# Kernel optimization log

Hardware: AMD Instinct MI355X
Metric: run time of the kernel (lower is better)

The kernel has to match this reference:

```python
import jax, jax.numpy as jnp
import numpy as np

B, C_IN, C_OUT, C_KEY, N = 8, 512, 512, 256, 2048


def setup_inputs() -> dict:
    key = jax.random.key(0)
    k1, k2, k3, k4 = jax.random.split(key, 4)
    x = jax.random.normal(k1, (B, C_IN, N), dtype=jnp.float32)
    # Conv1d(kernel=1, bias=False) weights -> plain linear maps over channel dim
    Wq = jax.random.normal(k2, (C_KEY, C_IN), dtype=jnp.float32) * (1.0 / np.sqrt(C_IN))
    Wk = jax.random.normal(k3, (C_KEY, C_IN), dtype=jnp.float32) * (1.0 / np.sqrt(C_IN))
    Wv = jax.random.normal(k4, (C_OUT, C_IN), dtype=jnp.float32) * (1.0 / np.sqrt(C_IN))
    return {"x": x, "Wq": Wq, "Wk": Wk, "Wv": Wv}


def reference(x, Wq, Wk, Wv):
    # 1x1 conv projections: [B, C, N] -> [B, Ck/Co, N]
    q = jnp.einsum("oc,bcn->bon", Wq, x)
    k = jnp.einsum("oc,bcn->bon", Wk, x)
    v = jnpqv = jnp.einsum("oc,bcn->bon", Wv, x)
    # sim_map[b,i,j] = sum_c k[b,c,i] * q[b,c,j]  (unscaled)
    sim = jnp.einsum("bci,bcj->bij", k, q)  # [B, N, N]
    attn = jax.nn.softmax(sim, axis=-1)
    # out = value @ sim_map, then permute(0,2,1) -> [B, N, C_out]
    out = jnp.einsum("bck,bkm->bmc", jnpqv, attn)
    return out
```

## Files before the change

kernel.cpp:

```cpp
#include <hip/hip_runtime.h>

typedef _Float16 half8 __attribute__((ext_vector_type(8)));
typedef _Float16 half4v __attribute__((ext_vector_type(4)));
typedef _Float16 half2v __attribute__((ext_vector_type(2)));
typedef float f32x4 __attribute__((ext_vector_type(4)));

#define ASYNC_CP16(gp, lp)                                       \
  __builtin_amdgcn_global_load_lds(                              \
      (const __attribute__((address_space(1))) void*)(gp),       \
      (__attribute__((address_space(3))) void*)(lp), 16, 0, 0)

static __device__ __forceinline__ half8 mulw(half8 a, half8 s) {
  half8 o;
#pragma unroll
  for (int j = 0; j < 8; j++) o[j] = a[j] * s[j];
  return o;
}

__global__ __launch_bounds__(256) void conv_w(const float* __restrict__ Wq,
                                              const float* __restrict__ Wk,
                                              const float* __restrict__ Wv,
                                              _Float16* __restrict__ Wb) {
  int idx = blockIdx.x * 256 + threadIdx.x;
  int row = idx >> 9;
  float v;
  if (row < 256)      v = Wq[idx];
  else if (row < 512) v = Wk[idx - 256 * 512];
  else                v = Wv[idx - 512 * 512];
  Wb[idx] = (_Float16)v;
}

__global__ __launch_bounds__(256) void conv_xT(const float* __restrict__ x,
                                               _Float16* __restrict__ xT) {
  __shared__ float T[32][33];
  const int b = blockIdx.z;
  const int n0 = blockIdx.x * 32, c0 = blockIdx.y * 32;
  const int t = threadIdx.x;
  const float* xb = x + (size_t)b * 512 * 2048;
  const int n2 = t & 15, cr = t >> 4;
#pragma unroll
  for (int r = 0; r < 2; r++) {
    int c = cr + r * 16;
    float2 v = *(const float2*)&xb[(size_t)(c0 + c) * 2048 + n0 + n2 * 2];
    T[c][n2 * 2] = v.x;
    T[c][n2 * 2 + 1] = v.y;
  }
  __syncthreads();
  _Float16* xtb = xT + (size_t)b * 2048 * 512;
  const int c2 = t & 15, nr = t >> 4;
#pragma unroll
  for (int r = 0; r < 2; r++) {
    int n = nr + r * 16;
    half2v h;
    h[0] = (_Float16)T[c2 * 2][n];
    h[1] = (_Float16)T[c2 * 2 + 1][n];
    *(half2v*)&xtb[(size_t)(n0 + n) * 512 + c0 + c2 * 2] = h;
  }
}

#define STAGE_NT(bb, kbase)                                   \
  ASYNC_CP16(gA + (kbase), &As[bb][0][wofs]);                 \
  ASYNC_CP16(gA + (kbase) + 32, &As[bb][1][wofs]);            \
  ASYNC_CP16(gB + (kbase), &Bs[bb][0][wofs]);                 \
  ASYNC_CP16(gB2 + (kbase), &Bs[bb][0][4096 + wofs]);         \
  ASYNC_CP16(gB + (kbase) + 32, &Bs[bb][1][wofs]);            \
  ASYNC_CP16(gB2 + (kbase) + 32, &Bs[bb][1][4096 + wofs]);

template <int MODE, int NT>
__global__ __launch_bounds__(512) void gemm_nt(
    const _Float16* __restrict__ A, const _Float16* __restrict__ B,
    _Float16* __restrict__ C, _Float16* __restrict__ C2, int lda, int ldb,
    int ldc, int ldc2, long sA, long sB, long sC, float* __restrict__ pm,
    float* __restrict__ ps) {
  A += (size_t)blockIdx.z * sA;
  B += (size_t)blockIdx.z * sB;
  C += (size_t)blockIdx.z * sC;
  if constexpr (MODE == 1) C2 += (size_t)blockIdx.z * sC;
  const int m_blk = blockIdx.y * 128, n_blk = blockIdx.x * 256;

  __shared__ __align__(16) _Float16 As[3][2][4096];
  __shared__ __align__(16) _Float16 Bs[3][2][8192];

  const int t = threadIdx.x;
  const int lane = t & 63, wave = t >> 6;
  const int quad = lane >> 4, l16 = lane & 15;
  const int wm = (wave & 1) * 64, wn = (wave >> 1) * 64;

  const int arow = t >> 2, aslot = t & 3;
  const int adc = aslot ^ ((arow >> 1) & 3);
  const _Float16* gA = A + (size_t)(m_blk + arow) * lda + adc * 8;
  const _Float16* gB = B + (size_t)(n_blk + arow) * ldb + adc * 8;
  const _Float16* gB2 = gB + (size_t)128 * ldb;
  const int wofs = wave * 512 + lane * 8;

  const int rchunk = (quad ^ ((l16 >> 1) & 3)) * 8;

  f32x4 acc[4][4] = {};

  STAGE_NT(0, 0);
  STAGE_NT(1, 64);
  asm volatile("s_waitcnt vmcnt(6)\n\ts_barrier" ::: "memory");
  __builtin_amdgcn_sched_barrier(0);

  int cbuf = 0;
  for (int T = 0; T < NT; T++) {
    const int kb2 = (T + 2) * 64;
    half8 af[4], bf[4];
#pragma unroll
    for (int i = 0; i < 4; i++) {
      af[i] = *(const half8*)&As[cbuf][0][(wm + i * 16 + l16) * 32 + rchunk];
      bf[i] = *(const half8*)&Bs[cbuf][0][(wn + i * 16 + l16) * 32 + rchunk];
    }
    if (T + 2 < NT) {
      int nb = cbuf + 2;
      if (nb >= 3) nb -= 3;
      STAGE_NT(nb, kb2);
    }
    asm volatile("s_barrier" ::: "memory");
    __builtin_amdgcn_sched_barrier(0);
    __builtin_amdgcn_s_setprio(1);
#pragma unroll
    for (int i = 0; i < 4; i++)
#pragma unroll
      for (int j = 0; j < 4; j++)
        acc[i][j] =
            __builtin_amdgcn_mfma_f32_16x16x32_f16(af[i], bf[j], acc[i][j], 0, 0, 0);
    __builtin_amdgcn_s_setprio(0);
    asm volatile("s_barrier" ::: "memory");
    __builtin_amdgcn_sched_barrier(0);
    half8 af2[4], bf2[4];
#pragma unroll
    for (int i = 0; i < 4; i++) {
      af2[i] = *(const half8*)&As[cbuf][1][(wm + i * 16 + l16) * 32 + rchunk];
      bf2[i] = *(const half8*)&Bs[cbuf][1][(wn + i * 16 + l16) * 32 + rchunk];
    }
    if (T + 2 < NT)
      asm volatile("s_waitcnt vmcnt(6)\n\ts_barrier" ::: "memory");
    else
      asm volatile("s_waitcnt vmcnt(0)\n\ts_barrier" ::: "memory");
    __builtin_amdgcn_sched_barrier(0);
    __builtin_amdgcn_s_setprio(1);
#pragma unroll
    for (int i = 0; i < 4; i++)
#pragma unroll
      for (int j = 0; j < 4; j++)
        acc[i][j] =
            __builtin_amdgcn_mfma_f32_16x16x32_f16(af2[i], bf2[j], acc[i][j], 0, 0, 0);
    __builtin_amdgcn_s_setprio(0);
    asm volatile("s_barrier" ::: "memory");
    __builtin_amdgcn_sched_barrier(0);
    cbuf++;
    if (cbuf == 3) cbuf = 0;
  }

  if constexpr (MODE == 2) {
#pragma unroll
    for (int j = 0; j < 4; j++) {
      const int n0 = n_blk + wn + j * 16 + l16;
      float mx = acc[0][j][0];
#pragma unroll
      for (int i = 0; i < 4; i++)
#pragma unroll
        for (int r = 0; r < 4; r++) mx = fmaxf(mx, acc[i][j][r]);
      mx = fmaxf(mx, __shfl_xor(mx, 16, 64));
      mx = fmaxf(mx, __shfl_xor(mx, 32, 64));
      float es = 0.f;
#pragma unroll
      for (int i = 0; i < 4; i++) {
        const int m0 = m_blk + wm + i * 16 + quad * 4;
#pragma unroll
        for (int r = 0; r < 4; r++) {
          _Float16 h = (_Float16)__expf(acc[i][j][r] - mx);
          C[(size_t)(m0 + r) * ldc + n0] = h;
          es += (float)h;
        }
      }
      es += __shfl_xor(es, 16, 64);
      es += __shfl_xor(es, 32, 64);
      if (quad == 0) {
        size_t o = ((size_t)blockIdx.z * 32 + blockIdx.y * 2 + (wave & 1)) *
                       2048 + n0;
        pm[o] = mx;
        ps[o] = es;
      }
    }
  } else {
#pragma unroll
    for (int i = 0; i < 4; i++) {
      const int m0 = m_blk + wm + i * 16 + quad * 4;
#pragma unroll
      for (int j = 0; j < 4; j++) {
        const int n0 = n_blk + wn + j * 16 + l16;
        if (m_blk < 512) {
          half4v h;
#pragma unroll
          for (int r = 0; r < 4; r++) h[r] = (_Float16)acc[i][j][r];
          *(half4v*)&C[(size_t)n0 * ldc + m0] = h;
        } else {
#pragma unroll
          for (int r = 0; r < 4; r++)
            C2[(size_t)(m0 - 512 + r) * ldc2 + n0] = (_Float16)acc[i][j][r];
        }
      }
    }
  }
}

__global__ __launch_bounds__(256) void colstats2(const float* __restrict__ pm,
                                                 const float* __restrict__ ps,
                                                 _Float16* __restrict__ scl) {
  const int idx = blockIdx.x * 256 + threadIdx.x;
  const int b = idx >> 11, col = idx & 2047;
  const float* pmb = pm + (size_t)b * 32 * 2048 + col;
  const float* psb = ps + (size_t)b * 32 * 2048 + col;
  float pv[32];
  float m = -3.0e38f;
#pragma unroll
  for (int i = 0; i < 32; i++) {
    pv[i] = pmb[(size_t)i * 2048];
    m = fmaxf(m, pv[i]);
  }
  float s = 0.f;
#pragma unroll
  for (int i = 0; i < 32; i++) {
    pv[i] = __expf(pv[i] - m);
    s += psb[(size_t)i * 2048] * pv[i];
  }
  const float inv = 1.0f / s;
  _Float16* so = scl + (size_t)b * 32 * 2048 + col;
#pragma unroll
  for (int i = 0; i < 32; i++) so[(size_t)i * 2048] = (_Float16)(pv[i] * inv);
}

__global__ __launch_bounds__(512) void gemm_av(const _Float16* __restrict__ P,
                                               const _Float16* __restrict__ V,
                                               const _Float16* __restrict__ scl,
                                               float* __restrict__ C,
                                               int cbatch) {
  int lin = blockIdx.x, z, idx;
  if (cbatch == 8) {
    z = lin & 7;
    idx = lin >> 3;
  } else {
    z = lin >> 5;
    idx = lin & 31;
  }
  const int n_blk = (idx & 1) * 256;
  const int m_blk = (idx >> 1) * 128;
  P += (size_t)z * 2048 * 2048;
  V += (size_t)z * 512 * 2048;
  scl += (size_t)z * 32 * 2048;
  C += (size_t)z * 2048 * 512;

  __shared__ __align__(16) _Float16 Asv[2][2][4096];
  __shared__ __align__(16) _Float16 Bsv[2][2][8192];

  const int t = threadIdx.x;
  const int lane = t & 63, wave = t >> 6;
  const int quad = lane >> 4, l16 = lane & 15;
  const int wm = (wave & 1) * 64, wn = (wave >> 1) * 64;

  const int arow = t >> 2;
  const int aslot = t & 3;
  const int adc = aslot ^ ((arow >> 1) & 3);
  const _Float16* gA = P + (size_t)(m_blk + arow) * 2048 + adc * 8;
  const _Float16* gS = scl + (size_t)((m_blk + arow) >> 6) * 2048 + adc * 8;
  const int awofs = arow * 32 + aslot * 8;

  const int brow0 = (wave << 4) + (lane >> 2);
  const int bdc = (lane & 3) ^ ((brow0 >> 1) & 3);
  const _Float16* gB = V + (size_t)(n_blk + brow0) * 2048 + bdc * 8;
  const int bwofs = wave << 9;

  const int rchunk = (quad ^ ((l16 >> 1) & 3)) * 8;

  f32x4 acc[4][4] = {};

  ASYNC_CP16(gB, &Bsv[0][0][bwofs]);
  ASYNC_CP16(gB + (size_t)128 * 2048, &Bsv[0][0][4096 + bwofs]);
  ASYNC_CP16(gB + 32, &Bsv[0][1][bwofs]);
  ASYNC_CP16(gB + (size_t)128 * 2048 + 32, &Bsv[0][1][4096 + bwofs]);
  {
    half8 a00 = *(const half8*)(gA);
    half8 s00 = *(const half8*)(gS);
    half8 a01 = *(const half8*)(gA + 32);
    half8 s01 = *(const half8*)(gS + 32);
    *(half8*)&Asv[0][0][awofs] = mulw(a00, s00);
    *(half8*)&Asv[0][1][awofs] = mulw(a01, s01);
  }
  half8 pA0 = *(const half8*)(gA + 64);
  half8 pS0 = *(const half8*)(gS + 64);
  half8 pA1 = *(const half8*)(gA + 96);
  half8 pS1 = *(const half8*)(gS + 96);
  asm volatile("s_waitcnt vmcnt(4) lgkmcnt(0)\n\ts_barrier" ::: "memory");
  __builtin_amdgcn_sched_barrier(0);

  for (int T = 0; T < 32; T++) {
    const int c = T & 1, n = c ^ 1;
    const int k1 = (T + 1) * 64;
    const int k2 = (T + 2) * 64;
    half8 af[4], bf[4];
#pragma unroll
    for (int i = 0; i < 4; i++) {
      af[i] = *(const half8*)&Asv[c][0][(wm + i * 16 + l16) * 32 + rchunk];
      bf[i] = *(const half8*)&Bsv[c][0][(wn + i * 16 + l16) * 32 + rchunk];
    }
    if (T < 31) {
      ASYNC_CP16(gB + k1, &Bsv[n][0][bwofs]);
      ASYNC_CP16(gB + (size_t)128 * 2048 + k1, &Bsv[n][0][4096 + bwofs]);
      ASYNC_CP16(gB + k1 + 32, &Bsv[n][1][bwofs]);
      ASYNC_CP16(gB + (size_t)128 * 2048 + k1 + 32, &Bsv[n][1][4096 + bwofs]);
      *(half8*)&Asv[n][0][awofs] = mulw(pA0, pS0);
    }
    asm volatile("s_barrier" ::: "memory");
    __builtin_amdgcn_sched_barrier(0);
    __builtin_amdgcn_s_setprio(1);
#pragma unroll
    for (int i = 0; i < 4; i++)
#pragma unroll
      for (int j = 0; j < 4; j++)
        acc[i][j] =
            __builtin_amdgcn_mfma_f32_16x16x32_f16(af[i], bf[j], acc[i][j], 0, 0, 0);
    __builtin_amdgcn_s_setprio(0);
    asm volatile("s_barrier" ::: "memory");
    __builtin_amdgcn_sched_barrier(0);
    half8 af2[4], bf2[4];
#pragma unroll
    for (int i = 0; i < 4; i++) {
      af2[i] = *(const half8*)&Asv[c][1][(wm + i * 16 + l16) * 32 + rchunk];
      bf2[i] = *(const half8*)&Bsv[c][1][(wn + i * 16 + l16) * 32 + rchunk];
    }
    half8 fA0, fS0, fA1, fS1;
    if (T < 30) {
      fA0 = *(const half8*)(gA + k2);
      fS0 = *(const half8*)(gS + k2);
      fA1 = *(const half8*)(gA + k2 + 32);
      fS1 = *(const half8*)(gS + k2 + 32);
    }
    if (T < 31) *(half8*)&Asv[n][1][awofs] = mulw(pA1, pS1);
    if (T < 30) {
      pA0 = fA0;
      pS0 = fS0;
      pA1 = fA1;
      pS1 = fS1;
    }
    if (T < 30)
      asm volatile("s_waitcnt vmcnt(4) lgkmcnt(0)\n\ts_barrier" ::: "memory");
    else
      asm volatile("s_waitcnt vmcnt(0) lgkmcnt(0)\n\ts_barrier" ::: "memory");
    __builtin_amdgcn_sched_barrier(0);
    __builtin_amdgcn_s_setprio(1);
#pragma unroll
    for (int i = 0; i < 4; i++)
#pragma unroll
      for (int j = 0; j < 4; j++)
        acc[i][j] =
            __builtin_amdgcn_mfma_f32_16x16x32_f16(af2[i], bf2[j], acc[i][j], 0, 0, 0);
    __builtin_amdgcn_s_setprio(0);
    asm volatile("s_barrier" ::: "memory");
    __builtin_amdgcn_sched_barrier(0);
  }

#pragma unroll
  for (int i = 0; i < 4; i++) {
    const int m0 = m_blk + wm + i * 16 + quad * 4;
#pragma unroll
    for (int j = 0; j < 4; j++) {
      const int n0 = n_blk + wn + j * 16 + l16;
#pragma unroll
      for (int r = 0; r < 4; r++) C[(size_t)(m0 + r) * 512 + n0] = acc[i][j][r];
    }
  }
}

extern "C" void kernel_launch(void* const* d_in, const int* in_sizes, int n_in,
                              void* d_out, int out_size, void* d_ws,
                              size_t ws_size, hipStream_t stream) {
  const float* x = (const float*)d_in[0];
  const float* Wq = (const float*)d_in[1];
  const float* Wk = (const float*)d_in[2];
  const float* Wv = (const float*)d_in[3];
  float* out = (float*)d_out;

  char* p = (char*)d_ws;
  auto alloc = [&](size_t bytes) -> char* {
    char* r = p;
    p += (bytes + 255) & ~(size_t)255;
    return r;
  };
  const size_t NB = 8, N = 2048, CIN = 512, CO = 512;
  _Float16* Wb = (_Float16*)alloc(1024 * 512 * sizeof(_Float16));
  _Float16* xT = (_Float16*)alloc(NB * N * CIN * sizeof(_Float16));
  _Float16* qkT = (_Float16*)alloc(NB * N * 512 * sizeof(_Float16));
  _Float16* v = (_Float16*)alloc(NB * CO * N * sizeof(_Float16));
  size_t base_used = (size_t)(p - (char*)d_ws);

  const size_t per_b =
      (size_t)N * N * 2 + 2 * 32 * N * 4 + 32 * N * 2 + 8192;
  int cb = 8;
  while (cb > 1 && base_used + (size_t)cb * per_b > ws_size) cb >>= 1;
  _Float16* simH = (_Float16*)alloc((size_t)cb * N * N * 2);
  float* pm = (float*)alloc((size_t)cb * 32 * N * 4);
  float* ps = (float*)alloc((size_t)cb * 32 * N * 4);
  _Float16* scl = (_Float16*)alloc((size_t)cb * 32 * N * 2);

  conv_w<<<dim3(1024 * 512 / 256), 256, 0, stream>>>(Wq, Wk, Wv, Wb);
  conv_xT<<<dim3(64, 16, 8), 256, 0, stream>>>(x, xT);

  gemm_nt<1, 8><<<dim3(8, 8, 8), 512, 0, stream>>>(
      Wb, xT, qkT, v, 512, 512, 512, 2048, 0, (long)(N * CIN),
      (long)(N * 512), nullptr, nullptr);

  for (int b0 = 0; b0 < 8; b0 += cb) {
    const _Float16* qT = qkT + (size_t)b0 * N * 512;
    const _Float16* kT = qkT + (size_t)b0 * N * 512 + 256;
    gemm_nt<2, 4><<<dim3(8, 16, cb), 512, 0, stream>>>(
        qT, kT, simH, nullptr, 512, 512, 2048, 0, (long)(N * 512),
        (long)(N * 512), (long)(N * N), pm, ps);
    colstats2<<<dim3(cb * 8), 256, 0, stream>>>(pm, ps, scl);
    gemm_av<<<dim3(32 * cb), 512, 0, stream>>>(
        simH, v + (size_t)b0 * CO * N, scl, out + (size_t)b0 * N * CO, cb);
  }
}
```

Baseline: 202.9 us.

## Split sim GEMM into dedicated 128x128-tile kernel with 256 threads

The similarity GEMM (K=256) gets its own kernel instead of sharing the templated projection GEMM. It uses 128x128 tiles with 4 waves, a simpler triple-buffered async LDS pipeline and twice as many blocks. The goal is better occupancy and load balance on a short-K GEMM, at the cost of less operand reuse per block. The fused exp and column-stat epilogue is kept unchanged.

```diff
diff --git a/kernel.cpp b/kernel.cpp
--- a/kernel.cpp
+++ b/kernel.cpp
@@ -66,16 +66,15 @@
   ASYNC_CP16(gB + (kbase) + 32, &Bs[bb][1][wofs]);            \
   ASYNC_CP16(gB2 + (kbase) + 32, &Bs[bb][1][4096 + wofs]);
 
-template <int MODE, int NT>
-__global__ __launch_bounds__(512) void gemm_nt(
+template <int NT>
+__global__ __launch_bounds__(512) void gemm_proj(
     const _Float16* __restrict__ A, const _Float16* __restrict__ B,
     _Float16* __restrict__ C, _Float16* __restrict__ C2, int lda, int ldb,
-    int ldc, int ldc2, long sA, long sB, long sC, float* __restrict__ pm,
-    float* __restrict__ ps) {
+    int ldc, int ldc2, long sA, long sB, long sC) {
   A += (size_t)blockIdx.z * sA;
   B += (size_t)blockIdx.z * sB;
   C += (size_t)blockIdx.z * sC;
-  if constexpr (MODE == 1) C2 += (size_t)blockIdx.z * sC;
+  C2 += (size_t)blockIdx.z * sC;
   const int m_blk = blockIdx.y * 128, n_blk = blockIdx.x * 256;
 
   __shared__ __align__(16) _Float16 As[3][2][4096];
@@ -153,55 +152,122 @@
     if (cbuf == 3) cbuf = 0;
   }
 
-  if constexpr (MODE == 2) {
+#pragma unroll
+  for (int i = 0; i < 4; i++) {
+    const int m0 = m_blk + wm + i * 16 + quad * 4;
 #pragma unroll
     for (int j = 0; j < 4; j++) {
       const int n0 = n_blk + wn + j * 16 + l16;
-      float mx = acc[0][j][0];
-#pragma unroll
-      for (int i = 0; i < 4; i++)
-#pragma unroll
-        for (int r = 0; r < 4; r++) mx = fmaxf(mx, acc[i][j][r]);
-      mx = fmaxf(mx, __shfl_xor(mx, 16, 64));
-      mx = fmaxf(mx, __shfl_xor(mx, 32, 64));
-      float es = 0.f;
-#pragma unroll
-      for (int i = 0; i < 4; i++) {
-        const int m0 = m_blk + wm + i * 16 + quad * 4;
-#pragma unroll
-        for (int r = 0; r < 4; r++) {
-          _Float16 h = (_Float16)__expf(acc[i][j][r] - mx);
-          C[(size_t)(m0 + r) * ldc + n0] = h;
-          es += (float)h;
-        }
+      if (m_blk < 512) {
+        half4v h;
+#pragma unroll
+        for (int r = 0; r < 4; r++) h[r] = (_Float16)acc[i][j][r];
+        *(half4v*)&C[(size_t)n0 * ldc + m0] = h;
+      } else {
+#pragma unroll
+        for (int r = 0; r < 4; r++)
+          C2[(size_t)(m0 - 512 + r) * ldc2 + n0] = (_Float16)acc[i][j][r];
       }
-      es += __shfl_xor(es, 16, 64);
-      es += __shfl_xor(es, 32, 64);
-      if (quad == 0) {
-        size_t o = ((size_t)blockIdx.z * 32 + blockIdx.y * 2 + (wave & 1)) *
-                       2048 + n0;
-        pm[o] = mx;
-        ps[o] = es;
+    }
+  }
+}
+
+__global__ __launch_bounds__(256) void gemm_sim(
+    const _Float16* __restrict__ A, const _Float16* __restrict__ B,
+    _Float16* __restrict__ C, long sA, long sB, long sC,
+    float* __restrict__ pm, float* __restrict__ ps) {
+  A += (size_t)blockIdx.z * sA;
+  B += (size_t)blockIdx.z * sB;
+  C += (size_t)blockIdx.z * sC;
+  const int m_blk = blockIdx.y * 128, n_blk = blockIdx.x * 128;
+
+  __shared__ __align__(16) _Float16 As[3][4096];
+  __shared__ __align__(16) _Float16 Bs[3][4096];
+
+  const int t = threadIdx.x;
+  const int lane = t & 63, wave = t >> 6;
+  const int quad = lane >> 4, l16 = lane & 15;
+  const int wm = (wave & 1) * 64, wn = (wave >> 1) * 64;
+
+  const int srow = 16 * wave + (lane >> 2);
+  const int schunk = (lane & 3) ^ ((lane >> 3) & 3);
+  const _Float16* gA0 = A + (size_t)(m_blk + srow) * 512 + schunk * 8;
+  const _Float16* gA1 = gA0 + (size_t)64 * 512;
+  const _Float16* gB0 = B + (size_t)(n_blk + srow) * 512 + schunk * 8;
+  const _Float16* gB1 = gB0 + (size_t)64 * 512;
+  const int lofs = wave * 512 + lane * 8;
+
+  const int rchunk = (quad ^ ((l16 >> 1) & 3)) * 8;
+
+  f32x4 acc[4][4] = {};
+
+#pragma unroll
+  for (int pb = 0; pb < 2; pb++) {
+    ASYNC_CP16(gA0 + pb * 32, &As[pb][lofs]);
+    ASYNC_CP16(gA1 + pb * 32, &As[pb][lofs + 2048]);
+    ASYNC_CP16(gB0 + pb * 32, &Bs[pb][lofs]);
+    ASYNC_CP16(gB1 + pb * 32, &Bs[pb][lofs + 2048]);
+  }
+
+  int ib = 0;
+  for (int k0 = 0; k0 < 256; k0 += 32) {
+    if (k0 + 32 < 256)
+      asm volatile("s_waitcnt vmcnt(4)\n\ts_barrier" ::: "memory");
+    else
+      asm volatile("s_waitcnt vmcnt(0)\n\ts_barrier" ::: "memory");
+    if (k0 + 64 < 256) {
+      int nb = ib + 2;
+      if (nb >= 3) nb -= 3;
+      const int ko = k0 + 64;
+      ASYNC_CP16(gA0 + ko, &As[nb][lofs]);
+      ASYNC_CP16(gA1 + ko, &As[nb][lofs + 2048]);
+      ASYNC_CP16(gB0 + ko, &Bs[nb][lofs]);
+      ASYNC_CP16(gB1 + ko, &Bs[nb][lofs + 2048]);
+    }
+    half8 af[4], bf[4];
+#pragma unroll
+    for (int i = 0; i < 4; i++) {
+      af[i] = *(const half8*)&As[ib][(wm + i * 16 + l16) * 32 + rchunk];
+      bf[i] = *(const half8*)&Bs[ib][(wn + i * 16 + l16) * 32 + rchunk];
+    }
+#pragma unroll
+    for (int i = 0; i < 4; i++)
+#pragma unroll
+      for (int j = 0; j < 4; j++)
+        acc[i][j] =
+            __builtin_amdgcn_mfma_f32_16x16x32_f16(af[i], bf[j], acc[i][j], 0, 0, 0);
+    ib++;
+    if (ib == 3) ib = 0;
+  }
+
+#pragma unroll
+  for (int j = 0; j < 4; j++) {
+    const int n0 = n_blk + wn + j * 16 + l16;
+    float mx = acc[0][j][0];
+#pragma unroll
+    for (int i = 0; i < 4; i++)
+#pragma unroll
+      for (int r = 0; r < 4; r++) mx = fmaxf(mx, acc[i][j][r]);
+    mx = fmaxf(mx, __shfl_xor(mx, 16, 64));
+    mx = fmaxf(mx, __shfl_xor(mx, 32, 64));
+    float es = 0.f;
+#pragma unroll
+    for (int i = 0; i < 4; i++) {
+      const int m0 = m_blk + wm + i * 16 + quad * 4;
+#pragma unroll
+      for (int r = 0; r < 4; r++) {
+        _Float16 h = (_Float16)__expf(acc[i][j][r] - mx);
+        C[(size_t)(m0 + r) * 2048 + n0] = h;
+        es += (float)h;
       }
     }
-  } else {
-#pragma unroll
-    for (int i = 0; i < 4; i++) {
-      const int m0 = m_blk + wm + i * 16 + quad * 4;
-#pragma unroll
-      for (int j = 0; j < 4; j++) {
-        const int n0 = n_blk + wn + j * 16 + l16;
-        if (m_blk < 512) {
-          half4v h;
-#pragma unroll
-          for (int r = 0; r < 4; r++) h[r] = (_Float16)acc[i][j][r];
-          *(half4v*)&C[(size_t)n0 * ldc + m0] = h;
-        } else {
-#pragma unroll
-          for (int r = 0; r < 4; r++)
-            C2[(size_t)(m0 - 512 + r) * ldc2 + n0] = (_Float16)acc[i][j][r];
-        }
-      }
+    es += __shfl_xor(es, 16, 64);
+    es += __shfl_xor(es, 32, 64);
+    if (quad == 0) {
+      size_t o =
+          ((size_t)blockIdx.z * 32 + blockIdx.y * 2 + (wave & 1)) * 2048 + n0;
+      pm[o] = mx;
+      ps[o] = es;
     }
   }
 }
@@ -407,16 +473,15 @@
   conv_w<<<dim3(1024 * 512 / 256), 256, 0, stream>>>(Wq, Wk, Wv, Wb);
   conv_xT<<<dim3(64, 16, 8), 256, 0, stream>>>(x, xT);
 
-  gemm_nt<1, 8><<<dim3(8, 8, 8), 512, 0, stream>>>(
+  gemm_proj<8><<<dim3(8, 8, 8), 512, 0, stream>>>(
       Wb, xT, qkT, v, 512, 512, 512, 2048, 0, (long)(N * CIN),
-      (long)(N * 512), nullptr, nullptr);
+      (long)(N * 512));
 
   for (int b0 = 0; b0 < 8; b0 += cb) {
     const _Float16* qT = qkT + (size_t)b0 * N * 512;
     const _Float16* kT = qkT + (size_t)b0 * N * 512 + 256;
-    gemm_nt<2, 4><<<dim3(8, 16, cb), 512, 0, stream>>>(
-        qT, kT, simH, nullptr, 512, 512, 2048, 0, (long)(N * 512),
-        (long)(N * 512), (long)(N * N), pm, ps);
+    gemm_sim<<<dim3(16, 16, cb), 256, 0, stream>>>(
+        qT, kT, simH, (long)(N * 512), (long)(N * 512), (long)(N * N), pm, ps);
     colstats2<<<dim3(cb * 8), 256, 0, stream>>>(pm, ps, scl);
     gemm_av<<<dim3(32 * cb), 512, 0, stream>>>(
         simH, v + (size_t)b0 * CO * N, scl, out + (size_t)b0 * N * CO, cb);
```

After: 195.9 us. 1.04x faster.
